# Kernel tuning notes

Measured on AMD Instinct MI355X. Metric: run time of the kernel, lower is better.

The kernel has to match this reference:

```python
import jax, jax.numpy as jnp
import numpy as np

EPS = 1e-12   # F.normalize eps
COS_EPS = 1e-8  # F.cosine_similarity eps

B, S, V, D, P, L = 4, 2048, 64, 1024, 8, 24
H = D // 24            # prefix_transform bottleneck = 42
K = 2 * L * D          # 49152 output feature dim


def setup_inputs() -> dict:
    key = jax.random.key(0)
    ks = jax.random.split(key, 8)
    return {
        "prefix": jax.random.randint(ks[0], (B, V), 0, V),
        "ctx_embeds": jax.random.normal(ks[1], (B, S, D), jnp.float32),
        "tables": jax.random.normal(ks[2], (P, V, D), jnp.float32) * 0.02,
        "lora_prefix_emb": jax.random.normal(ks[3], (P, D), jnp.float32),
        "w1": jax.random.normal(ks[4], (D, H), jnp.float32) * 0.02,
        "b1": jnp.zeros((H,), jnp.float32),
        "w2": jax.random.normal(ks[5], (H, K), jnp.float32) * 0.02,
        "b2": jnp.zeros((K,), jnp.float32),
    }


def _gates(ctx_embeds, lora_prefix_emb):
    """select_prefix, vectorized over the num_prefix_set loop.

    The original builds sim_i = bmm(norm(emb), norm(e_i.repeat(B,S,1), dim=0).permute)
    of shape [B,S,S]; since the key is repeated, every column of sim is identical,
    so we carry the column vector [P,B,S] and the math is exact.
    """
    b, s, _ = ctx_embeds.shape
    # normalize embedding over feature dim (F.normalize p=2 dim=2)
    emb_n = ctx_embeds / jnp.maximum(
        jnp.linalg.norm(ctx_embeds, axis=2, keepdims=True), EPS)
    # F.normalize over dim=0 of a tensor repeated B times -> sign(x)/sqrt(B)
    u = lora_prefix_emb / jnp.maximum(
        jnp.sqrt(float(b)) * jnp.abs(lora_prefix_emb), EPS)  # [P,D]
    v = jnp.einsum('bsd,pd->pbs', emb_n, u)          # column of sim matrix
    c = jnp.maximum(v, 0.0)                          # clamp(min=0)
    # F.normalize over last dim (length S, all entries equal c) -> c/(sqrt(S)*c)
    n = c / jnp.maximum(jnp.sqrt(float(s)) * c, EPS)
    w = jax.nn.softmax(n, axis=2)                    # softmax over token dim (dim=1 in torch layout)
    a_v = jnp.einsum('pbs,bsd->pbd', w, ctx_embeds)  # attended value per expert
    e_norm = jnp.linalg.norm(lora_prefix_emb, axis=1)          # [P]
    a_norm = jnp.linalg.norm(a_v, axis=2)                      # [P,B]
    cos = jnp.einsum('pd,pbd->pb', lora_prefix_emb, a_v) / \
        jnp.maximum(e_norm[:, None] * a_norm, COS_EPS)
    return jax.nn.softmax(cos.T, axis=-1)            # self.s_t, [B,P]


def reference(prefix, ctx_embeds, tables, lora_prefix_emb, w1, b1, w2, b2):
    s_t = _gates(ctx_embeds, lora_prefix_emb)        # [B,P]
    # forward() re-applies softmax to self.s_t (faithful double softmax)
    gate = jax.nn.softmax(s_t, axis=-1)              # [B,P]
    tok = tables[:, prefix]                          # [P,B,V,D] per-expert embedding lookup
    h = jnp.tanh(jnp.einsum('pbvd,dh->pbvh', tok, w1) + b1)
    pkv = jnp.einsum('pbvh,hk->pbvk', h, w2) + b2    # [P,B,V,K]
    out = jnp.einsum('bp,pbvk->bvk', gate, pkv)      # gated mixture over experts
    return out
```

## Files before the change

kernel.cpp:

```cpp
#include <hip/hip_runtime.h>

#define BB 4
#define SS 2048
#define VV 64
#define DD 1024
#define PP 8
#define HH 42
#define KK 49152
#define NCHUNK 64

static constexpr float F_EPS = 1e-12f;
static constexpr float ALPHA = 1.02234304f;

__global__ __launch_bounds__(512) void kU(
    const float* __restrict__ ctx, const float* __restrict__ lora,
    float* __restrict__ part) {
  __shared__ float smem[PP * DD + 16 + 32 * PP];
  const int t = threadIdx.x;
  const int b = blockIdx.y;
  const int chunk = blockIdx.x;
  float* u_lds = smem;
  float* w_lds = smem + PP * DD + 16;
  {
    const float4* lora4 = (const float4*)lora;
    float4* u4w = (float4*)u_lds;
    #pragma unroll
    for (int i = t; i < PP * DD / 4; i += 512) {
      float4 e = lora4[i];
      float4 u;
      u.x = e.x / fmaxf(2.0f * fabsf(e.x), F_EPS);
      u.y = e.y / fmaxf(2.0f * fabsf(e.y), F_EPS);
      u.z = e.z / fmaxf(2.0f * fabsf(e.z), F_EPS);
      u.w = e.w / fmaxf(2.0f * fabsf(e.w), F_EPS);
      u4w[i] = u;
    }
  }
  __syncthreads();
  const int wave = t >> 6, lane = t & 63;
  const int rbase = b * SS + chunk * 32 + wave * 4;
  const float4* ctx4 = (const float4*)ctx;
  const float4* u4 = (const float4*)u_lds;
  float dot[4][PP];
  #pragma unroll
  for (int i = 0; i < 4; ++i)
    #pragma unroll
    for (int p = 0; p < PP; ++p) dot[i][p] = 0.f;
  #pragma unroll
  for (int j = 0; j < 4; ++j) {
    float4 c[4];
    #pragma unroll
    for (int i = 0; i < 4; ++i)
      c[i] = ctx4[(size_t)(rbase + i) * 256 + j * 64 + lane];
    #pragma unroll
    for (int p = 0; p < PP; ++p) {
      float4 u = u4[p * 256 + j * 64 + lane];
      #pragma unroll
      for (int i = 0; i < 4; ++i)
        dot[i][p] += c[i].x * u.x + c[i].y * u.y + c[i].z * u.z + c[i].w * u.w;
    }
  }
  const int sel = lane & 7;
  #pragma unroll
  for (int i = 0; i < 4; ++i) {
    float d0 = dot[i][0], d1 = dot[i][1], d2 = dot[i][2], d3 = dot[i][3];
    float d4 = dot[i][4], d5 = dot[i][5], d6 = dot[i][6], d7 = dot[i][7];
    #pragma unroll
    for (int m = 1; m <= 4; m <<= 1) {
      d0 += __shfl_xor(d0, m, 64); d1 += __shfl_xor(d1, m, 64);
      d2 += __shfl_xor(d2, m, 64); d3 += __shfl_xor(d3, m, 64);
      d4 += __shfl_xor(d4, m, 64); d5 += __shfl_xor(d5, m, 64);
      d6 += __shfl_xor(d6, m, 64); d7 += __shfl_xor(d7, m, 64);
    }
    float v = d0;
    v = (sel == 1) ? d1 : v; v = (sel == 2) ? d2 : v;
    v = (sel == 3) ? d3 : v; v = (sel == 4) ? d4 : v;
    v = (sel == 5) ? d5 : v; v = (sel == 6) ? d6 : v;
    v = (sel == 7) ? d7 : v;
    v += __shfl_xor(v, 8, 64);
    v += __shfl_xor(v, 16, 64);
    v += __shfl_xor(v, 32, 64);
    if (lane < PP)
      w_lds[(wave * 4 + i) * PP + lane] = (v > 0.0f) ? ALPHA : 1.0f;
  }
  __syncthreads();
  float2 acc[PP];
  #pragma unroll
  for (int p = 0; p < PP; ++p) acc[p] = make_float2(0.f, 0.f);
  const float2* ctx2 = (const float2*)ctx;
  const float4* w4 = (const float4*)w_lds;
  #pragma unroll 4
  for (int sl = 0; sl < 32; ++sl) {
    float2 c = ctx2[(size_t)(b * SS + chunk * 32 + sl) * 512 + t];
    float4 wa = w4[sl * 2];
    float4 wb = w4[sl * 2 + 1];
    float w[PP] = {wa.x, wa.y, wa.z, wa.w, wb.x, wb.y, wb.z, wb.w};
    #pragma unroll
    for (int p = 0; p < PP; ++p) {
      acc[p].x += w[p] * c.x;
      acc[p].y += w[p] * c.y;
    }
  }
  float2* part2 = (float2*)part;
  #pragma unroll
  for (int p = 0; p < PP; ++p)
    part2[(size_t)((b * NCHUNK + chunk) * PP + p) * 512 + t] = acc[p];
}

__global__ __launch_bounds__(512) void k4h(
    const float* __restrict__ part, const float* __restrict__ lora,
    const float* __restrict__ tables, const float* __restrict__ w1,
    const float* __restrict__ b1, float* __restrict__ cos_ws,
    float* __restrict__ h_all) {
  __shared__ float smem[DD + 512];
  const int t = threadIdx.x;
  if (blockIdx.x < 32) {
    const int p = blockIdx.x & 7, b = blockIdx.x >> 3;
    const float2* p2 = (const float2*)part;
    float avx = 0.f, avy = 0.f;
    #pragma unroll 8
    for (int c = 0; c < NCHUNK; ++c) {
      float2 x = p2[(size_t)((b * NCHUNK + c) * PP + p) * 512 + t];
      avx += x.x; avy += x.y;
    }
    float2 e = ((const float2*)lora)[p * 512 + t];
    float dt = avx * e.x + avy * e.y;
    float a2 = avx * avx + avy * avy;
    float e2 = e.x * e.x + e.y * e.y;
    #pragma unroll
    for (int m = 32; m >= 1; m >>= 1) {
      dt += __shfl_xor(dt, m, 64);
      a2 += __shfl_xor(a2, m, 64);
      e2 += __shfl_xor(e2, m, 64);
    }
    const int wave = t >> 6, lane = t & 63;
    if (lane == 0) {
      smem[wave * 3 + 0] = dt;
      smem[wave * 3 + 1] = a2;
      smem[wave * 3 + 2] = e2;
    }
    __syncthreads();
    if (t == 0) {
      float Dv = 0.f, Av = 0.f, Ev = 0.f;
      #pragma unroll
      for (int w8 = 0; w8 < 8; ++w8) {
        Dv += smem[w8 * 3 + 0];
        Av += smem[w8 * 3 + 1];
        Ev += smem[w8 * 3 + 2];
      }
      cos_ws[b * PP + p] = Dv / fmaxf(sqrtf(Ev) * sqrtf(Av), 1e-8f);
    }
  } else {
    float* row_lds = smem;
    float* partial = smem + DD;
    const int r = blockIdx.x - 32;
    ((float2*)row_lds)[t] = ((const float2*)(tables + (size_t)r * DD))[t];
    __syncthreads();
    const int h = t & 63, q = t >> 6;
    float acc = 0.0f;
    if (h < HH) {
      const int d0 = q * 128;
      #pragma unroll 8
      for (int dl = 0; dl < 128; ++dl) {
        acc += row_lds[d0 + dl] * w1[(size_t)(d0 + dl) * HH + h];
      }
    }
    partial[q * 64 + h] = acc;
    __syncthreads();
    if (t < HH) {
      float s = 0.0f;
      #pragma unroll
      for (int q8 = 0; q8 < 8; ++q8) s += partial[q8 * 64 + t];
      h_all[(size_t)r * HH + t] = tanhf(s + b1[t]);
    }
  }
}

__global__ __launch_bounds__(256) void k7_out(
    const float* __restrict__ w2, const float* __restrict__ b2,
    const float* __restrict__ h_all, const float* __restrict__ cos_ws,
    const int* __restrict__ prefix, float* __restrict__ out) {
  __shared__ float gate_lds[PP];
  __shared__ float hg_lds[HH * 64];
  __shared__ float w2_lds[HH * 128];
  const int t = threadIdx.x;
  const int b = blockIdx.y;
  const size_t kbase = (size_t)blockIdx.x * 128;
  for (int i = t; i < HH * 128; i += 256) {
    int h = i >> 7, kk = i & 127;
    w2_lds[i] = w2[(size_t)h * KK + kbase + kk];
  }
  if (t == 0) {
    float c[PP];
    float m = -1e30f;
    #pragma unroll
    for (int p = 0; p < PP; ++p) { c[p] = cos_ws[b * PP + p]; m = fmaxf(m, c[p]); }
    float s = 0.0f;
    #pragma unroll
    for (int p = 0; p < PP; ++p) { c[p] = expf(c[p] - m); s += c[p]; }
    float inv = 1.0f / s;
    float m2 = -1e30f;
    #pragma unroll
    for (int p = 0; p < PP; ++p) { c[p] *= inv; m2 = fmaxf(m2, c[p]); }
    float s2 = 0.0f;
    #pragma unroll
    for (int p = 0; p < PP; ++p) { c[p] = expf(c[p] - m2); s2 += c[p]; }
    float inv2 = 1.0f / s2;
    #pragma unroll
    for (int p = 0; p < PP; ++p) gate_lds[p] = c[p] * inv2;
  }
  __syncthreads();
  for (int idx = t; idx < 64 * HH; idx += 256) {
    int v = idx / HH;
    int h = idx - v * HH;
    int tokv = prefix[b * VV + v];
    float s = 0.0f;
    #pragma unroll
    for (int p = 0; p < PP; ++p)
      s += gate_lds[p] * h_all[(size_t)(p * VV + tokv) * HH + h];
    hg_lds[h * 64 + v] = s;
  }
  __syncthreads();
  const int tk = t & 31, tb = t >> 5;
  float4 acc[8];
  #pragma unroll
  for (int i = 0; i < 8; ++i) acc[i] = make_float4(0.f, 0.f, 0.f, 0.f);
  const float4* w24 = (const float4*)w2_lds;
  const float4* hg4 = (const float4*)hg_lds;
  #pragma unroll 2
  for (int h = 0; h < HH; ++h) {
    float4 wv = w24[h * 32 + tk];
    float4 g0 = hg4[h * 16 + tb * 2];
    float4 g1 = hg4[h * 16 + tb * 2 + 1];
    float gg[8] = {g0.x, g0.y, g0.z, g0.w, g1.x, g1.y, g1.z, g1.w};
    #pragma unroll
    for (int i = 0; i < 8; ++i) {
      acc[i].x += gg[i] * wv.x;
      acc[i].y += gg[i] * wv.y;
      acc[i].z += gg[i] * wv.z;
      acc[i].w += gg[i] * wv.w;
    }
  }
  float4 b2v = ((const float4*)b2)[(kbase >> 2) + tk];
  float4* out4 = (float4*)out;
  #pragma unroll
  for (int i = 0; i < 8; ++i) {
    int bv = b * 64 + tb * 8 + i;
    float4 o;
    o.x = acc[i].x + b2v.x;
    o.y = acc[i].y + b2v.y;
    o.z = acc[i].z + b2v.z;
    o.w = acc[i].w + b2v.w;
    out4[(((size_t)bv * KK + kbase) >> 2) + tk] = o;
  }
}

extern "C" void kernel_launch(void* const* d_in, const int* in_sizes, int n_in,
                              void* d_out, int out_size, void* d_ws, size_t ws_size,
                              hipStream_t stream) {
  const int* prefix = (const int*)d_in[0];
  const float* ctx = (const float*)d_in[1];
  const float* tables = (const float*)d_in[2];
  const float* lora = (const float*)d_in[3];
  const float* w1 = (const float*)d_in[4];
  const float* b1 = (const float*)d_in[5];
  const float* w2 = (const float*)d_in[6];
  const float* b2 = (const float*)d_in[7];
  float* out = (float*)d_out;
  char* ws = (char*)d_ws;
  float* part = (float*)ws;
  float* cos_ws = (float*)(ws + 8388608);
  float* h_all = (float*)(ws + 8388608 + 128);

  kU<<<dim3(64, 4), 512, 0, stream>>>(ctx, lora, part);
  k4h<<<dim3(32 + 512), 512, 0, stream>>>(part, lora, tables, w1, b1,
                                          cos_ws, h_all);
  k7_out<<<dim3(384, 4), 256, 0, stream>>>(w2, b2, h_all, cos_ws, prefix, out);
}
```

Before: 148.1 us.

## Process eight table rows per block in k4h; vectorize w2 staging, register gates

The table-row projection in k4h now handles 8 rows per block, so each w1 value is loaded once and reused across 8 rows, and the launch shrinks from 512 to 64 row blocks. k7_out now stages w2 into shared memory with float4 loads. Every thread computes the double-softmax gates in registers, which removes the shared gate array and one barrier. The cost is a larger shared-memory footprint and fewer blocks in k4h, which lowers parallelism on that stage.

```diff
diff --git a/kernel.cpp b/kernel.cpp
--- a/kernel.cpp
+++ b/kernel.cpp
@@ -111,7 +111,7 @@
     const float* __restrict__ tables, const float* __restrict__ w1,
     const float* __restrict__ b1, float* __restrict__ cos_ws,
     float* __restrict__ h_all) {
-  __shared__ float smem[DD + 512];
+  __shared__ float smem[8 * DD + 8 * 8 * 64];
   const int t = threadIdx.x;
   if (blockIdx.x < 32) {
     const int p = blockIdx.x & 7, b = blockIdx.x >> 3;
@@ -151,26 +151,38 @@
     }
   } else {
     float* row_lds = smem;
-    float* partial = smem + DD;
-    const int r = blockIdx.x - 32;
-    ((float2*)row_lds)[t] = ((const float2*)(tables + (size_t)r * DD))[t];
+    float* partial = smem + 8 * DD;
+    const int rbase = (blockIdx.x - 32) * 8;
+    {
+      const float4* src = (const float4*)(tables + (size_t)rbase * DD);
+      float4* dst = (float4*)row_lds;
+      #pragma unroll
+      for (int i = t; i < 8 * DD / 4; i += 512) dst[i] = src[i];
+    }
     __syncthreads();
     const int h = t & 63, q = t >> 6;
-    float acc = 0.0f;
+    float acc[8];
+    #pragma unroll
+    for (int r = 0; r < 8; ++r) acc[r] = 0.f;
     if (h < HH) {
       const int d0 = q * 128;
       #pragma unroll 8
       for (int dl = 0; dl < 128; ++dl) {
-        acc += row_lds[d0 + dl] * w1[(size_t)(d0 + dl) * HH + h];
+        float wv = w1[(size_t)(d0 + dl) * HH + h];
+        #pragma unroll
+        for (int r = 0; r < 8; ++r)
+          acc[r] += row_lds[r * DD + d0 + dl] * wv;
       }
     }
-    partial[q * 64 + h] = acc;
+    #pragma unroll
+    for (int r = 0; r < 8; ++r) partial[(q * 8 + r) * 64 + h] = acc[r];
     __syncthreads();
-    if (t < HH) {
+    const int r = t >> 6;
+    if (h < HH) {
       float s = 0.0f;
       #pragma unroll
-      for (int q8 = 0; q8 < 8; ++q8) s += partial[q8 * 64 + t];
-      h_all[(size_t)r * HH + t] = tanhf(s + b1[t]);
+      for (int q8 = 0; q8 < 8; ++q8) s += partial[(q8 * 8 + r) * 64 + h];
+      h_all[(size_t)(rbase + r) * HH + h] = tanhf(s + b1[h]);
     }
   }
 }
@@ -179,17 +191,21 @@
     const float* __restrict__ w2, const float* __restrict__ b2,
     const float* __restrict__ h_all, const float* __restrict__ cos_ws,
     const int* __restrict__ prefix, float* __restrict__ out) {
-  __shared__ float gate_lds[PP];
   __shared__ float hg_lds[HH * 64];
   __shared__ float w2_lds[HH * 128];
   const int t = threadIdx.x;
   const int b = blockIdx.y;
   const size_t kbase = (size_t)blockIdx.x * 128;
-  for (int i = t; i < HH * 128; i += 256) {
-    int h = i >> 7, kk = i & 127;
-    w2_lds[i] = w2[(size_t)h * KK + kbase + kk];
-  }
-  if (t == 0) {
+  {
+    const float4* w2g = (const float4*)w2;
+    float4* w2l = (float4*)w2_lds;
+    for (int i = t; i < HH * 32; i += 256) {
+      int h = i >> 5, k4 = i & 31;
+      w2l[i] = w2g[(size_t)h * (KK / 4) + (kbase >> 2) + k4];
+    }
+  }
+  float gate[PP];
+  {
     float c[PP];
     float m = -1e30f;
     #pragma unroll
@@ -206,9 +222,8 @@
     for (int p = 0; p < PP; ++p) { c[p] = expf(c[p] - m2); s2 += c[p]; }
     float inv2 = 1.0f / s2;
     #pragma unroll
-    for (int p = 0; p < PP; ++p) gate_lds[p] = c[p] * inv2;
-  }
-  __syncthreads();
+    for (int p = 0; p < PP; ++p) gate[p] = c[p] * inv2;
+  }
   for (int idx = t; idx < 64 * HH; idx += 256) {
     int v = idx / HH;
     int h = idx - v * HH;
@@ -216,7 +231,7 @@
     float s = 0.0f;
     #pragma unroll
     for (int p = 0; p < PP; ++p)
-      s += gate_lds[p] * h_all[(size_t)(p * VV + tokv) * HH + h];
+      s += gate[p] * h_all[(size_t)(p * VV + tokv) * HH + h];
     hg_lds[h * 64 + v] = s;
   }
   __syncthreads();
@@ -272,7 +287,7 @@
   float* h_all = (float*)(ws + 8388608 + 128);
 
   kU<<<dim3(64, 4), 512, 0, stream>>>(ctx, lora, part);
-  k4h<<<dim3(32 + 512), 512, 0, stream>>>(part, lora, tables, w1, b1,
-                                          cos_ws, h_all);
+  k4h<<<dim3(32 + 64), 512, 0, stream>>>(part, lora, tables, w1, b1,
+                                         cos_ws, h_all);
   k7_out<<<dim3(384, 4), 256, 0, stream>>>(w2, b2, h_all, cos_ws, prefix, out);
 }
```

Result: slower. 181.3 us (+22.4%).
